# Performance work log

Hardware: AMD Instinct MI355X
Metric: run time of the kernel (lower is better)

## Reference

```python
import jax, jax.numpy as jnp
import numpy as np

EMB_DIM = 512
NUM_HEADS = 8
SEQ_LEN = 4096
BATCH = 4


def setup_inputs() -> dict:
    key = jax.random.key(0)
    k = jax.random.split(key, 5)
    E = EMB_DIM
    scale = 1.0 / np.sqrt(E)
    x = jax.random.normal(k[0], (BATCH, SEQ_LEN, E), dtype=jnp.float32)
    Wqkv = jax.random.normal(k[1], (E, 3 * E), dtype=jnp.float32) * scale
    bqkv = jax.random.normal(k[2], (3 * E,), dtype=jnp.float32) * 0.01
    Wo = jax.random.normal(k[3], (E, E), dtype=jnp.float32) * scale
    bo = jax.random.normal(k[4], (E,), dtype=jnp.float32) * 0.01
    return {"x": x, "Wqkv": Wqkv, "bqkv": bqkv, "Wo": Wo, "bo": bo}


def reference(x, Wqkv, bqkv, Wo, bo):
    B, S, E = x.shape
    H = NUM_HEADS
    Dh = E // H
    qkv = x @ Wqkv + bqkv                      # [B,S,3E]
    q, k, v = jnp.split(qkv, 3, axis=-1)
    # [B,S,E] -> [B,H,S,Dh]
    q = q.reshape(B, S, H, Dh).transpose(0, 2, 1, 3)
    k = k.reshape(B, S, H, Dh).transpose(0, 2, 1, 3)
    v = v.reshape(B, S, H, Dh).transpose(0, 2, 1, 3)
    att = jnp.einsum("bhsd,bhtd->bhst", q, k) / jnp.sqrt(jnp.asarray(Dh, x.dtype))
    causal = jnp.tril(jnp.ones((S, S), dtype=bool))
    att = jnp.where(causal[None, None], att, -jnp.inf)
    att = jax.nn.softmax(att, axis=-1)
    out = jnp.einsum("bhst,bhtd->bhsd", att, v)  # [B,H,S,Dh]
    out = out.transpose(0, 2, 1, 3).reshape(B, S, E)
    return out @ Wo + bo
```

## Files before the change

kernel.cpp:

```cpp
#include <hip/hip_runtime.h>
#include <math.h>

#define NB 4
#define NS 4096
#define NE 512
#define NH 8
#define ND 64
#define N3 1536
#define NM (NB*NS)

typedef __attribute__((ext_vector_type(8))) short bf16x8;
typedef __attribute__((ext_vector_type(4))) float f32x4;
typedef unsigned short ushort_t;

__device__ __forceinline__ unsigned short f2bf(float f) {
    union { float f; unsigned int u; } v; v.f = f;
    unsigned int r = (v.u + 0x7FFFu + ((v.u >> 16) & 1u)) >> 16;
    return (unsigned short)r;
}

typedef __attribute__((address_space(1))) const void g_void;
typedef __attribute__((address_space(3))) void l_void;
__device__ __forceinline__ void cp16(const void* g, void* l) {
    __builtin_amdgcn_global_load_lds((g_void*)g, (l_void*)l, 16, 0, 0);
}

__global__ __launch_bounds__(256)
void cast_x(const float* __restrict__ x, ushort_t* __restrict__ xb) {
    const size_t i = ((size_t)blockIdx.x * 256 + threadIdx.x) * 4;
    float4 v = *(const float4*)&x[i];
    ushort4 o;
    o.x = f2bf(v.x); o.y = f2bf(v.y); o.z = f2bf(v.z); o.w = f2bf(v.w);
    *(ushort4*)&xb[i] = o;
}

__global__ __launch_bounds__(256)
void cast_wT(const float* __restrict__ W, ushort_t* __restrict__ WT, int N) {
    __shared__ ushort_t T[64][72];
    const int t = threadIdx.x;
    const int k0 = blockIdx.y * 64, n0 = blockIdx.x * 64;
    const int tx = t & 15, ty = t >> 4;
    #pragma unroll
    for (int p = 0; p < 4; ++p) {
        const int r = p * 16 + ty;
        float4 v = *(const float4*)&W[(size_t)(k0 + r) * N + n0 + tx * 4];
        T[tx*4+0][r] = f2bf(v.x);
        T[tx*4+1][r] = f2bf(v.y);
        T[tx*4+2][r] = f2bf(v.z);
        T[tx*4+3][r] = f2bf(v.w);
    }
    __syncthreads();
    const int nn = t >> 2, kc = (t & 3) * 16;
    uint4 a = *(uint4*)&T[nn][kc];
    uint4 b = *(uint4*)&T[nn][kc + 8];
    *(uint4*)&WT[(size_t)(n0 + nn) * 512 + k0 + kc]     = a;
    *(uint4*)&WT[(size_t)(n0 + nn) * 512 + k0 + kc + 8] = b;
}

__global__ __launch_bounds__(256)
void qkv_mfma(const ushort_t* __restrict__ xb, const ushort_t* __restrict__ WT,
              const float* __restrict__ bqkv,
              ushort_t* __restrict__ Qb, ushort_t* __restrict__ Kb,
              ushort_t* __restrict__ Vb)
{
    __shared__ ushort_t As[128 * 32];
    __shared__ ushort_t Bs[128 * 32];
    const int tid = threadIdx.x;
    const int lane = tid & 63, w = tid >> 6;
    const int col = lane & 15, quad = lane >> 4;
    const int wm = w & 1, wn = w >> 1;
    const int m0 = blockIdx.y * 128;
    const int nblk = blockIdx.x * 128;

    const int arow = tid >> 2, ach = (tid & 3) * 8;
    const ushort_t* aSrc = xb + (size_t)(m0 + arow) * 512 + ach;
    const ushort_t* bSrc = WT + (size_t)(nblk + arow) * 512 + ach;
    ushort_t* aDst = As + tid * 8;
    ushort_t* bDst = Bs + tid * 8;

    f32x4 acc[4][4];
    #pragma unroll
    for (int i = 0; i < 4; ++i)
        #pragma unroll
        for (int j = 0; j < 4; ++j)
            #pragma unroll
            for (int r = 0; r < 4; ++r) acc[i][j][r] = 0.f;

    for (int k0 = 0; k0 < 512; k0 += 32) {
        __syncthreads();
        cp16(aSrc + k0, aDst);
        cp16(aSrc + 64 * 512 + k0, aDst + 2048);
        cp16(bSrc + k0, bDst);
        cp16(bSrc + 64 * 512 + k0, bDst + 2048);
        __syncthreads();
        bf16x8 af[4], bf[4];
        #pragma unroll
        for (int mt = 0; mt < 4; ++mt)
            af[mt] = *(const bf16x8*)&As[(wm*64 + mt*16 + col) * 32 + quad*8];
        #pragma unroll
        for (int nt = 0; nt < 4; ++nt)
            bf[nt] = *(const bf16x8*)&Bs[(wn*64 + nt*16 + col) * 32 + quad*8];
        #pragma unroll
        for (int nt = 0; nt < 4; ++nt)
            #pragma unroll
            for (int mt = 0; mt < 4; ++mt)
                acc[mt][nt] = __builtin_amdgcn_mfma_f32_16x16x32_bf16(
                    af[mt], bf[nt], acc[mt][nt], 0, 0, 0);
    }

    const int which = nblk >> 9;
    const float scale = (which == 0) ? 0.125f : 1.0f;
    const int b = m0 >> 12;
    const int s0 = m0 & (NS - 1);
    float bias[4];
    int hh[4], dd[4];
    #pragma unroll
    for (int nt = 0; nt < 4; ++nt) {
        const int n = nblk + wn*64 + nt*16 + col;
        bias[nt] = bqkv[n];
        const int e = n & (NE - 1);
        hh[nt] = e >> 6; dd[nt] = e & 63;
    }
    if (which == 2) {
        #pragma unroll
        for (int mt = 0; mt < 4; ++mt)
            #pragma unroll
            for (int reg = 0; reg < 4; ++reg) {
                const int s = s0 + wm*64 + mt*16 + quad*4 + reg;
                #pragma unroll
                for (int nt = 0; nt < 4; ++nt)
                    Vb[((size_t)(b*NH + hh[nt]) * ND + dd[nt]) * NS + s] =
                        f2bf(acc[mt][nt][reg] + bias[nt]);
            }
    } else {
        ushort_t* dst = (which == 0) ? Qb : Kb;
        #pragma unroll
        for (int mt = 0; mt < 4; ++mt)
            #pragma unroll
            for (int reg = 0; reg < 4; ++reg) {
                const int s = s0 + wm*64 + mt*16 + quad*4 + reg;
                #pragma unroll
                for (int nt = 0; nt < 4; ++nt)
                    dst[((size_t)(b*NH + hh[nt]) * NS + s) * ND + dd[nt]] =
                        f2bf((acc[mt][nt][reg] + bias[nt]) * scale);
            }
    }
}

__global__ __launch_bounds__(256)
void flash_mfma(const ushort_t* __restrict__ Qb,
                const ushort_t* __restrict__ Kb,
                const ushort_t* __restrict__ Vb,
                ushort_t* __restrict__ Ob)
{
    __shared__ __align__(16) ushort_t Ks[64][72];
    __shared__ __align__(16) ushort_t VT[64][72];
    __shared__ __align__(16) ushort_t Ps[4][32][72];

    const int tid  = threadIdx.x;
    const int w    = tid >> 6;
    const int lane = tid & 63;
    const int col  = lane & 15;
    const int quad = lane >> 4;
    const int qpair = blockIdx.x;
    const int bh   = blockIdx.y;
    const size_t base = (size_t)bh * NS * ND;

    bf16x8 ones;
    {
        const short o = (col == 0) ? (short)0x3F80 : (short)0;
        #pragma unroll
        for (int j = 0; j < 8; ++j) ones[j] = o;
    }

    #pragma unroll 1
    for (int phase = 0; phase < 2; ++phase) {
        const int qv = phase ? (31 - qpair) : qpair;

        bf16x8 aq[2][2];
        #pragma unroll
        for (int mt = 0; mt < 2; ++mt)
            #pragma unroll
            for (int kh = 0; kh < 2; ++kh)
                aq[mt][kh] = *(const bf16x8*)
                    &Qb[base + (size_t)(qv*128 + w*32 + mt*16 + col) * ND
                        + kh*32 + quad*8];

        f32x4 acc[2][4];
        f32x4 lacc[2];
        #pragma unroll
        for (int mt = 0; mt < 2; ++mt) {
            #pragma unroll
            for (int r = 0; r < 4; ++r) lacc[mt][r] = 0.f;
            #pragma unroll
            for (int nt = 0; nt < 4; ++nt)
                #pragma unroll
                for (int r = 0; r < 4; ++r) acc[mt][nt][r] = 0.f;
        }

        const int nkt = 2 * qv + 2;
        for (int kt = 0; kt < nkt; ++kt) {
            __syncthreads();
            {
                const int r = tid & 63;
                const int dg = tid >> 6;
                const ushort_t* ksrc = &Kb[base + (size_t)(kt*64 + r) * ND + dg*16];
                *(uint4*)&Ks[r][dg*16]     = *(const uint4*)ksrc;
                *(uint4*)&Ks[r][dg*16 + 8] = *(const uint4*)(ksrc + 8);
                const ushort_t* vsrc = &Vb[base + (size_t)r * NS + kt*64 + dg*16];
                *(uint4*)&VT[r][dg*16]     = *(const uint4*)vsrc;
                *(uint4*)&VT[r][dg*16 + 8] = *(const uint4*)(vsrc + 8);
            }
            __syncthreads();

            if (kt*64 >= qv*128 + w*32 + 32) continue;

            f32x4 s[2][4];
            #pragma unroll
            for (int mt = 0; mt < 2; ++mt)
                #pragma unroll
                for (int nt = 0; nt < 4; ++nt)
                    #pragma unroll
                    for (int r = 0; r < 4; ++r) s[mt][nt][r] = 0.f;

            #pragma unroll
            for (int nt = 0; nt < 4; ++nt)
                #pragma unroll
                for (int kh = 0; kh < 2; ++kh) {
                    bf16x8 ak = *(const bf16x8*)&Ks[nt*16 + col][kh*32 + quad*8];
                    #pragma unroll
                    for (int mt = 0; mt < 2; ++mt)
                        s[mt][nt] = __builtin_amdgcn_mfma_f32_16x16x32_bf16(
                            ak, aq[mt][kh], s[mt][nt], 0, 0, 0);
                }

            if (kt >= 2 * qv) {
                #pragma unroll
                for (int mt = 0; mt < 2; ++mt) {
                    const int qrow = qv*128 + w*32 + mt*16 + col;
                    #pragma unroll
                    for (int nt = 0; nt < 4; ++nt) {
                        const int key = kt*64 + nt*16 + quad*4;
                        #pragma unroll
                        for (int reg = 0; reg < 4; ++reg)
                            if (key + reg > qrow) s[mt][nt][reg] = -1e30f;
                    }
                }
            }

            #pragma unroll
            for (int mt = 0; mt < 2; ++mt)
                #pragma unroll
                for (int nt = 0; nt < 4; ++nt) {
                    ushort4 pw;
                    pw.x = f2bf(__expf(s[mt][nt][0]));
                    pw.y = f2bf(__expf(s[mt][nt][1]));
                    pw.z = f2bf(__expf(s[mt][nt][2]));
                    pw.w = f2bf(__expf(s[mt][nt][3]));
                    *(ushort4*)&Ps[w][mt*16 + col][nt*16 + quad*4] = pw;
                }

            bf16x8 ap[2][2];
            #pragma unroll
            for (int mt = 0; mt < 2; ++mt)
                #pragma unroll
                for (int kh = 0; kh < 2; ++kh)
                    ap[mt][kh] = *(const bf16x8*)&Ps[w][mt*16 + col][kh*32 + quad*8];

            #pragma unroll
            for (int mt = 0; mt < 2; ++mt)
                #pragma unroll
                for (int kh = 0; kh < 2; ++kh)
                    lacc[mt] = __builtin_amdgcn_mfma_f32_16x16x32_bf16(
                        ap[mt][kh], ones, lacc[mt], 0, 0, 0);

            #pragma unroll
            for (int nt = 0; nt < 4; ++nt)
                #pragma unroll
                for (int kh = 0; kh < 2; ++kh) {
                    bf16x8 bv = *(const bf16x8*)&VT[nt*16 + col][kh*32 + quad*8];
                    #pragma unroll
                    for (int mt = 0; mt < 2; ++mt)
                        acc[mt][nt] = __builtin_amdgcn_mfma_f32_16x16x32_bf16(
                            ap[mt][kh], bv, acc[mt][nt], 0, 0, 0);
                }
        }

        #pragma unroll
        for (int mt = 0; mt < 2; ++mt)
            #pragma unroll
            for (int reg = 0; reg < 4; ++reg) {
                const float l = __shfl(lacc[mt][reg], lane & 48, 64);
                const float inv = 1.f / l;
                const int row = qv*128 + w*32 + mt*16 + quad*4 + reg;
                #pragma unroll
                for (int nt = 0; nt < 4; ++nt)
                    Ob[base + (size_t)row * ND + nt*16 + col] =
                        f2bf(acc[mt][nt][reg] * inv);
            }
        __syncthreads();
    }
}

__global__ __launch_bounds__(256)
void out_mfma(const ushort_t* __restrict__ Ob, const ushort_t* __restrict__ WT,
              const float* __restrict__ bo, float* __restrict__ out)
{
    __shared__ ushort_t As[128 * 32];
    __shared__ ushort_t Bs[128 * 32];
    const int tid = threadIdx.x;
    const int lane = tid & 63, w = tid >> 6;
    const int col = lane & 15, quad = lane >> 4;
    const int wm = w & 1, wn = w >> 1;
    const int m0 = blockIdx.y * 128;
    const int nblk = blockIdx.x * 128;

    const int arow = tid >> 2, ach = (tid & 3) * 8;
    const int bblk = m0 >> 12;
    const int s0 = m0 & (NS - 1);
    const ushort_t* bSrc = WT + (size_t)(nblk + arow) * 512 + ach;
    ushort_t* aDst = As + tid * 8;
    ushort_t* bDst = Bs + tid * 8;

    f32x4 acc[4][4];
    #pragma unroll
    for (int i = 0; i < 4; ++i)
        #pragma unroll
        for (int j = 0; j < 4; ++j)
            #pragma unroll
            for (int r = 0; r < 4; ++r) acc[i][j][r] = 0.f;

    for (int k0 = 0; k0 < 512; k0 += 32) {
        __syncthreads();
        const int h = k0 >> 6, koff = k0 & 63;
        const ushort_t* aS =
            Ob + ((size_t)(bblk*NH + h) * NS + s0 + arow) * ND + koff + ach;
        cp16(aS, aDst);
        cp16(aS + 64 * ND, aDst + 2048);
        cp16(bSrc + k0, bDst);
        cp16(bSrc + 64 * 512 + k0, bDst + 2048);
        __syncthreads();
        bf16x8 af[4], bf[4];
        #pragma unroll
        for (int mt = 0; mt < 4; ++mt)
            af[mt] = *(const bf16x8*)&As[(wm*64 + mt*16 + col) * 32 + quad*8];
        #pragma unroll
        for (int nt = 0; nt < 4; ++nt)
            bf[nt] = *(const bf16x8*)&Bs[(wn*64 + nt*16 + col) * 32 + quad*8];
        #pragma unroll
        for (int nt = 0; nt < 4; ++nt)
            #pragma unroll
            for (int mt = 0; mt < 4; ++mt)
                acc[mt][nt] = __builtin_amdgcn_mfma_f32_16x16x32_bf16(
                    af[mt], bf[nt], acc[mt][nt], 0, 0, 0);
    }

    float bias[4];
    #pragma unroll
    for (int nt = 0; nt < 4; ++nt)
        bias[nt] = bo[nblk + wn*64 + nt*16 + col];
    #pragma unroll
    for (int mt = 0; mt < 4; ++mt)
        #pragma unroll
        for (int reg = 0; reg < 4; ++reg) {
            const int m = m0 + wm*64 + mt*16 + quad*4 + reg;
            #pragma unroll
            for (int nt = 0; nt < 4; ++nt)
                out[(size_t)m * NE + nblk + wn*64 + nt*16 + col] =
                    acc[mt][nt][reg] + bias[nt];
        }
}

extern "C" void kernel_launch(void* const* d_in, const int* in_sizes, int n_in,
                              void* d_out, int out_size, void* d_ws, size_t ws_size,
                              hipStream_t stream) {
    const float* x    = (const float*)d_in[0];
    const float* Wqkv = (const float*)d_in[1];
    const float* bqkv = (const float*)d_in[2];
    const float* Wo   = (const float*)d_in[3];
    const float* bo   = (const float*)d_in[4];
    float* out = (float*)d_out;

    const size_t per = (size_t)NB * NH * NS * ND;
    ushort_t* ws = (ushort_t*)d_ws;
    ushort_t* xb     = ws;
    ushort_t* Ob     = ws;
    ushort_t* Qb     = ws + per;
    ushort_t* Kb     = Qb + per;
    ushort_t* Vb     = Kb + per;
    ushort_t* WqkvT  = Vb + per;
    ushort_t* WoT    = WqkvT + (size_t)N3 * NE;

    dim3 blk(256);
    cast_x<<<dim3(NM * NE / 1024), blk, 0, stream>>>(x, xb);
    cast_wT<<<dim3(N3/64, NE/64), blk, 0, stream>>>(Wqkv, WqkvT, N3);
    cast_wT<<<dim3(NE/64, NE/64), blk, 0, stream>>>(Wo, WoT, NE);
    qkv_mfma<<<dim3(N3/128, NM/128), blk, 0, stream>>>(xb, WqkvT, bqkv, Qb, Kb, Vb);
    flash_mfma<<<dim3(16, NB*NH), blk, 0, stream>>>(Qb, Kb, Vb, Ob);
    out_mfma<<<dim3(NE/128, NM/128), blk, 0, stream>>>(Ob, WoT, bo, out);
}
```

Before: 292.2 us.

## Prefetch K/V tiles into registers, use exp2 with folded scale and packed bf16 convert

```diff
diff --git a/kernel.cpp b/kernel.cpp
--- a/kernel.cpp
+++ b/kernel.cpp
@@ -13,12 +13,34 @@
 typedef __attribute__((ext_vector_type(4))) float f32x4;
 typedef unsigned short ushort_t;
 
+#define QSCALE 0.18033688011f
+
+extern "C" __device__ float __ocml_native_exp2_f32(float);
+
 __device__ __forceinline__ unsigned short f2bf(float f) {
     union { float f; unsigned int u; } v; v.f = f;
     unsigned int r = (v.u + 0x7FFFu + ((v.u >> 16) & 1u)) >> 16;
     return (unsigned short)r;
 }
 
+#if defined(__has_builtin)
+#if __has_builtin(__builtin_amdgcn_cvt_pk_bf16_f32)
+#define HAVE_PK_BF16 1
+#endif
+#endif
+
+#ifdef HAVE_PK_BF16
+typedef __attribute__((ext_vector_type(2))) __bf16 bf16x2_t;
+__device__ __forceinline__ unsigned int pk2bf(float a, float b) {
+    bf16x2_t r = __builtin_amdgcn_cvt_pk_bf16_f32(a, b);
+    union { bf16x2_t v; unsigned int u; } c; c.v = r; return c.u;
+}
+#else
+__device__ __forceinline__ unsigned int pk2bf(float a, float b) {
+    return (unsigned int)f2bf(a) | ((unsigned int)f2bf(b) << 16);
+}
+#endif
+
 typedef __attribute__((address_space(1))) const void g_void;
 typedef __attribute__((address_space(3))) void l_void;
 __device__ __forceinline__ void cp16(const void* g, void* l) {
@@ -29,9 +51,10 @@
 void cast_x(const float* __restrict__ x, ushort_t* __restrict__ xb) {
     const size_t i = ((size_t)blockIdx.x * 256 + threadIdx.x) * 4;
     float4 v = *(const float4*)&x[i];
-    ushort4 o;
-    o.x = f2bf(v.x); o.y = f2bf(v.y); o.z = f2bf(v.z); o.w = f2bf(v.w);
-    *(ushort4*)&xb[i] = o;
+    uint2 o;
+    o.x = pk2bf(v.x, v.y);
+    o.y = pk2bf(v.z, v.w);
+    *(uint2*)&xb[i] = o;
 }
 
 __global__ __launch_bounds__(256)
@@ -109,7 +132,7 @@
     }
 
     const int which = nblk >> 9;
-    const float scale = (which == 0) ? 0.125f : 1.0f;
+    const float scale = (which == 0) ? QSCALE : 1.0f;
     const int b = m0 >> 12;
     const int s0 = m0 & (NS - 1);
     float bias[4];
@@ -166,6 +189,11 @@
     const int bh   = blockIdx.y;
     const size_t base = (size_t)bh * NS * ND;
 
+    const int r  = tid & 63;
+    const int dg = tid >> 6;
+    const ushort_t* kbase = Kb + base + (size_t)r * ND + dg*16;
+    const ushort_t* vbase = Vb + base + (size_t)r * NS + dg*16;
+
     bf16x8 ones;
     {
         const short o = (col == 0) ? (short)0x3F80 : (short)0;
@@ -191,27 +219,41 @@
         #pragma unroll
         for (int mt = 0; mt < 2; ++mt) {
             #pragma unroll
-            for (int r = 0; r < 4; ++r) lacc[mt][r] = 0.f;
+            for (int r2 = 0; r2 < 4; ++r2) lacc[mt][r2] = 0.f;
             #pragma unroll
             for (int nt = 0; nt < 4; ++nt)
                 #pragma unroll
-                for (int r = 0; r < 4; ++r) acc[mt][nt][r] = 0.f;
+                for (int r2 = 0; r2 < 4; ++r2) acc[mt][nt][r2] = 0.f;
         }
 
         const int nkt = 2 * qv + 2;
+
+        uint4 kr0, kr1, vr0, vr1;
+        {
+            const ushort_t* ks = kbase;
+            kr0 = *(const uint4*)ks;
+            kr1 = *(const uint4*)(ks + 8);
+            const ushort_t* vs = vbase;
+            vr0 = *(const uint4*)vs;
+            vr1 = *(const uint4*)(vs + 8);
+        }
+
         for (int kt = 0; kt < nkt; ++kt) {
             __syncthreads();
-            {
-                const int r = tid & 63;
-                const int dg = tid >> 6;
-                const ushort_t* ksrc = &Kb[base + (size_t)(kt*64 + r) * ND + dg*16];
-                *(uint4*)&Ks[r][dg*16]     = *(const uint4*)ksrc;
-                *(uint4*)&Ks[r][dg*16 + 8] = *(const uint4*)(ksrc + 8);
-                const ushort_t* vsrc = &Vb[base + (size_t)r * NS + kt*64 + dg*16];
-                *(uint4*)&VT[r][dg*16]     = *(const uint4*)vsrc;
-                *(uint4*)&VT[r][dg*16 + 8] = *(const uint4*)(vsrc + 8);
+            *(uint4*)&Ks[r][dg*16]     = kr0;
+            *(uint4*)&Ks[r][dg*16 + 8] = kr1;
+            *(uint4*)&VT[r][dg*16]     = vr0;
+            *(uint4*)&VT[r][dg*16 + 8] = vr1;
+            __syncthreads();
+
+            if (kt + 1 < nkt) {
+                const ushort_t* ks = kbase + (size_t)(kt+1) * 64 * ND;
+                kr0 = *(const uint4*)ks;
+                kr1 = *(const uint4*)(ks + 8);
+                const ushort_t* vs = vbase + (kt+1) * 64;
+                vr0 = *(const uint4*)vs;
+                vr1 = *(const uint4*)(vs + 8);
             }
-            __syncthreads();
 
             if (kt*64 >= qv*128 + w*32 + 32) continue;
 
@@ -221,7 +263,7 @@
                 #pragma unroll
                 for (int nt = 0; nt < 4; ++nt)
                     #pragma unroll
-                    for (int r = 0; r < 4; ++r) s[mt][nt][r] = 0.f;
+                    for (int r2 = 0; r2 < 4; ++r2) s[mt][nt][r2] = 0.f;
 
             #pragma unroll
             for (int nt = 0; nt < 4; ++nt)
@@ -252,12 +294,12 @@
             for (int mt = 0; mt < 2; ++mt)
                 #pragma unroll
                 for (int nt = 0; nt < 4; ++nt) {
-                    ushort4 pw;
-                    pw.x = f2bf(__expf(s[mt][nt][0]));
-                    pw.y = f2bf(__expf(s[mt][nt][1]));
-                    pw.z = f2bf(__expf(s[mt][nt][2]));
-                    pw.w = f2bf(__expf(s[mt][nt][3]));
-                    *(ushort4*)&Ps[w][mt*16 + col][nt*16 + quad*4] = pw;
+                    uint2 pw;
+                    pw.x = pk2bf(__ocml_native_exp2_f32(s[mt][nt][0]),
+                                 __ocml_native_exp2_f32(s[mt][nt][1]));
+                    pw.y = pk2bf(__ocml_native_exp2_f32(s[mt][nt][2]),
+                                 __ocml_native_exp2_f32(s[mt][nt][3]));
+                    *(uint2*)&Ps[w][mt*16 + col][nt*16 + quad*4] = pw;
                 }
 
             bf16x8 ap[2][2];
@@ -298,7 +340,6 @@
                     Ob[base + (size_t)row * ND + nt*16 + col] =
                         f2bf(acc[mt][nt][reg] * inv);
             }
-        __syncthreads();
     }
 }
 
```

Result: faster. 275.0 us (-5.9%).
